# Performance work log

Measured on AMD Instinct MI355X. Metric: run time of the kernel, lower is better.

The kernel has to match this reference:

```python
import jax, jax.numpy as jnp
import numpy as np

NUM_EMBEDDINGS = 1024
EMBEDDING_DIM = 64
COMMIT_COST = 0.25


def setup_inputs() -> dict:
    key = jax.random.key(0)
    k1, k2 = jax.random.split(key)
    latent = jax.random.normal(k1, (32, EMBEDDING_DIM, 32, 32), dtype=jnp.float32)
    embedding_weight = jax.random.normal(k2, (NUM_EMBEDDINGS, EMBEDDING_DIM), dtype=jnp.float32)
    return {"latent": latent, "embedding_weight": embedding_weight}


def reference(latent, embedding_weight):
    # rearrange 'b n j d -> b j d n'; n == embedding_dim
    lat = jnp.transpose(latent, (0, 2, 3, 1))  # [b, j, d, n]
    flat = lat.reshape(-1, EMBEDDING_DIM)      # [T, D]
    # squared-euclidean distances [T, K]
    distances = (
        jnp.sum(flat ** 2, axis=1, keepdims=True)
        + jnp.sum(embedding_weight ** 2, axis=1)
        - 2.0 * flat @ embedding_weight.T
    )
    idx = jnp.argmin(distances, axis=1)                         # [T]
    encodings = jax.nn.one_hot(idx, NUM_EMBEDDINGS, dtype=flat.dtype)  # [T, K]
    quantized_flat = embedding_weight[idx]                      # gather == encodings @ W
    quantized = quantized_flat.reshape(lat.shape)               # [b, j, d, n]

    e_latent_loss = jnp.mean((jax.lax.stop_gradient(quantized) - lat) ** 2)
    loss = COMMIT_COST * e_latent_loss

    # straight-through estimator
    quantized_st = lat + jax.lax.stop_gradient(quantized - lat)

    avg_probs = jnp.mean(encodings, axis=0)
    perplexity = jnp.exp(-jnp.sum(avg_probs * jnp.log(avg_probs + 1e-10)))

    # rearrange back 'b j d n -> b n j d'
    quantized_out = jnp.transpose(quantized_st, (0, 3, 1, 2))
    return quantized_out, loss, perplexity, encodings, distances
```

## Files before the change

### kernel.cpp

```cpp
#include <hip/hip_runtime.h>
#include <cfloat>

#define T_TOTAL 32768
#define DIM 64
#define KCODES 1024

static constexpr long long OFF_Q    = 0;
static constexpr long long OFF_LOSS = 2097152;
static constexpr long long OFF_PERP = 2097153;
static constexpr long long OFF_ENC  = 2097154;
static constexpr long long OFF_DIST = 2097154LL + 33554432LL;


__global__ __launch_bounds__(256) void vq_prep_kernel(const float* __restrict__ W,
                                                      float* __restrict__ ww,
                                                      float* __restrict__ WT) {
    const int tid = threadIdx.x;
    if (blockIdx.x < 256) {
        const int lane = tid & 63;
        const int code = blockIdx.x * 4 + (tid >> 6);
        float v = W[code * DIM + lane];
        float s = v * v;
        #pragma unroll
        for (int off = 32; off > 0; off >>= 1)
            s += __shfl_down(s, off, 64);
        if (lane == 0) ww[code] = s;
    } else {
        const int n = blockIdx.x - 256;
        #pragma unroll
        for (int i = 0; i < 4; ++i) {
            int k = i * 256 + tid;
            WT[n * KCODES + k] = W[k * DIM + n];
        }
    }
}

__global__ __launch_bounds__(256, 3) void vq_main_kernel(const float* __restrict__ lat,
                                                         const float* __restrict__ W,
                                                         const float* __restrict__ ww,
                                                         const float* __restrict__ WT,
                                                         float* __restrict__ out,
                                                         int* __restrict__ counts,
                                                         float* __restrict__ lossSum) {
    __shared__ float xT[64 * 64];
    __shared__ float wS[32 * 256];
    __shared__ float xx[64];
    __shared__ int   selIdx[64];

    const int tid = threadIdx.x;
    const int tx  = tid & 31;
    const int ty  = tid >> 5;
    const int t0  = blockIdx.x * 64;
    const long long base = (long long)(t0 >> 10) * 65536 + (long long)(t0 & 1023);

    #pragma unroll
    for (int i = 0; i < 16; ++i) {
        int e  = i * 256 + tid;
        int n  = e >> 6;
        int tl = e & 63;
        xT[n * 64 + tl] = lat[base + (long long)n * 1024 + tl];
    }
    __syncthreads();
    if (tid < 64) {
        float s = 0.f;
        #pragma unroll 8
        for (int n = 0; n < 64; ++n) {
            float v = xT[n * 64 + tid];
            s = fmaf(v, v, s);
        }
        xx[tid] = s;
    }

    float minV[8];
    int   minI[8];
    #pragma unroll
    for (int r = 0; r < 8; ++r) { minV[r] = FLT_MAX; minI[r] = 0; }

    float* __restrict__ distOut = out + OFF_DIST;

    for (int c = 0; c < 4; ++c) {
        float acc[8][8];
        #pragma unroll
        for (int r = 0; r < 8; ++r)
            #pragma unroll
            for (int k = 0; k < 8; ++k) acc[r][k] = 0.f;

        for (int h = 0; h < 2; ++h) {
            __syncthreads();
            #pragma unroll
            for (int i = 0; i < 8; ++i) {
                int e2 = i * 256 + tid;
                int n  = e2 >> 6;
                int k4 = e2 & 63;
                *(float4*)&wS[n * 256 + k4 * 4] =
                    *(const float4*)&WT[(h * 32 + n) * KCODES + c * 256 + k4 * 4];
            }
            __syncthreads();

            #pragma unroll 4
            for (int nn = 0; nn < 32; ++nn) {
                const float* xrow = &xT[(h * 32 + nn) * 64];
                const float* wrow = &wS[nn * 256];
                float4 a0 = *(const float4*)&xrow[ty * 4];
                float4 a1 = *(const float4*)&xrow[32 + ty * 4];
                float4 b0 = *(const float4*)&wrow[tx * 4];
                float4 b1 = *(const float4*)&wrow[128 + tx * 4];
                float ar[8] = {a0.x, a0.y, a0.z, a0.w, a1.x, a1.y, a1.z, a1.w};
                float br[8] = {b0.x, b0.y, b0.z, b0.w, b1.x, b1.y, b1.z, b1.w};
                #pragma unroll
                for (int r = 0; r < 8; ++r)
                    #pragma unroll
                    for (int k = 0; k < 8; ++k)
                        acc[r][k] = fmaf(ar[r], br[k], acc[r][k]);
            }
        }

        const int kb0 = c * 256 + tx * 4;
        float wr[8];
        #pragma unroll
        for (int k = 0; k < 8; ++k)
            wr[k] = ww[kb0 + (k >> 2) * 128 + (k & 3)];
        #pragma unroll
        for (int r = 0; r < 8; ++r) {
            const int row = (r >> 2) * 32 + ty * 4 + (r & 3);
            const float xxr = xx[row];
            float d[8];
            #pragma unroll
            for (int k = 0; k < 8; ++k) {
                d[k] = (xxr + wr[k]) - 2.f * acc[r][k];
                int ki = kb0 + (k >> 2) * 128 + (k & 3);
                if (d[k] < minV[r]) { minV[r] = d[k]; minI[r] = ki; }
            }
            const long long ro = (long long)(t0 + row) * KCODES + kb0;
            *(float2*)&distOut[ro]           = make_float2(d[0], d[1]);
            *(float2*)&distOut[ro + 2]       = make_float2(d[2], d[3]);
            *(float2*)&distOut[ro + 128]     = make_float2(d[4], d[5]);
            *(float2*)&distOut[ro + 130]     = make_float2(d[6], d[7]);
        }
    }

    __syncthreads();
    float* redV = wS;
    int*   redI = (int*)(wS + 64 * 33);
    #pragma unroll
    for (int r = 0; r < 8; ++r) {
        const int row = (r >> 2) * 32 + ty * 4 + (r & 3);
        redV[row * 33 + tx] = minV[r];
        redI[row * 33 + tx] = minI[r];
    }
    __syncthreads();
    if (tid < 64) {
        float best = redV[tid * 33];
        int   bi   = redI[tid * 33];
        #pragma unroll
        for (int s = 1; s < 32; ++s) {
            float v  = redV[tid * 33 + s];
            int   i2 = redI[tid * 33 + s];
            if (v < best || (v == best && i2 < bi)) { best = v; bi = i2; }
        }
        selIdx[tid] = bi;
        atomicAdd(&counts[bi], 1);
    }
    __syncthreads();

    float* qS = wS;
    #pragma unroll
    for (int i = 0; i < 16; ++i) {
        int e   = i * 256 + tid;
        int row = e >> 6;
        int n   = e & 63;
        qS[row * 65 + n] = W[selIdx[row] * DIM + n];
    }
    __syncthreads();

    float ls = 0.f;
    #pragma unroll
    for (int i = 0; i < 4; ++i) {
        int e2  = i * 256 + tid;
        int n   = e2 >> 4;
        int tl0 = (e2 & 15) * 4;
        float q0 = qS[(tl0 + 0) * 65 + n];
        float q1 = qS[(tl0 + 1) * 65 + n];
        float q2 = qS[(tl0 + 2) * 65 + n];
        float q3 = qS[(tl0 + 3) * 65 + n];
        float x0 = xT[n * 64 + tl0 + 0];
        float x1 = xT[n * 64 + tl0 + 1];
        float x2 = xT[n * 64 + tl0 + 2];
        float x3 = xT[n * 64 + tl0 + 3];
        *(float4*)&out[OFF_Q + base + (long long)n * 1024 + tl0] = make_float4(q0, q1, q2, q3);
        float e0 = q0 - x0; ls = fmaf(e0, e0, ls);
        float e1 = q1 - x1; ls = fmaf(e1, e1, ls);
        float e2d = q2 - x2; ls = fmaf(e2d, e2d, ls);
        float e3 = q3 - x3; ls = fmaf(e3, e3, ls);
    }
    #pragma unroll
    for (int off = 32; off > 0; off >>= 1)
        ls += __shfl_down(ls, off, 64);
    if ((tid & 63) == 0) atomicAdd(lossSum, ls);

    float* __restrict__ enc = out + OFF_ENC;
    for (int i = 0; i < 128; ++i) {
        int e2  = i * 256 + tid;
        int row = e2 >> 9;
        int k2  = (e2 & 511) * 2;
        int sel = selIdx[row];
        float2 v;
        v.x = (k2     == sel) ? 1.f : 0.f;
        v.y = (k2 + 1 == sel) ? 1.f : 0.f;
        *(float2*)&enc[(long long)(t0 + row) * KCODES + k2] = v;
    }
}

__global__ __launch_bounds__(1024) void vq_finalize_kernel(const int* __restrict__ counts,
                                                           const float* __restrict__ lossSum,
                                                           float* __restrict__ out) {
    __shared__ float red[16];
    const int tid = threadIdx.x;
    float p = (float)counts[tid] * (1.0f / 32768.0f);
    float term = p * logf(p + 1e-10f);
    #pragma unroll
    for (int off = 32; off > 0; off >>= 1)
        term += __shfl_down(term, off, 64);
    if ((tid & 63) == 0) red[tid >> 6] = term;
    __syncthreads();
    if (tid == 0) {
        float s = 0.f;
        #pragma unroll
        for (int i = 0; i < 16; ++i) s += red[i];
        out[OFF_PERP] = expf(-s);
        out[OFF_LOSS] = 0.25f * lossSum[0] * (1.0f / 2097152.0f);
    }
}

extern "C" void kernel_launch(void* const* d_in, const int* in_sizes, int n_in,
                              void* d_out, int out_size, void* d_ws, size_t ws_size,
                              hipStream_t stream) {
    (void)in_sizes; (void)n_in; (void)out_size; (void)ws_size;
    const float* lat = (const float*)d_in[0];
    const float* W   = (const float*)d_in[1];
    float* out = (float*)d_out;

    int*   counts  = (int*)d_ws;
    float* ww      = (float*)((char*)d_ws + 4096);
    float* lossSum = (float*)((char*)d_ws + 8192);
    float* WT      = (float*)((char*)d_ws + 12288);

    hipMemsetAsync(d_ws, 0, 8192 + 16, stream);

    vq_prep_kernel<<<320, 256, 0, stream>>>(W, ww, WT);
    vq_main_kernel<<<512, 256, 0, stream>>>(lat, W, ww, WT, out, counts, lossSum);
    vq_finalize_kernel<<<1, 1024, 0, stream>>>(counts, lossSum, out);
}
```

Baseline: 340.2 us.

## Retile VQ main kernel to 32 tokens per block with wave-level argmin

```diff
diff --git a/kernel.cpp b/kernel.cpp
--- a/kernel.cpp
+++ b/kernel.cpp
@@ -35,37 +35,37 @@
     }
 }
 
-__global__ __launch_bounds__(256, 3) void vq_main_kernel(const float* __restrict__ lat,
+__global__ __launch_bounds__(256, 4) void vq_main_kernel(const float* __restrict__ lat,
                                                          const float* __restrict__ W,
                                                          const float* __restrict__ ww,
                                                          const float* __restrict__ WT,
                                                          float* __restrict__ out,
                                                          int* __restrict__ counts,
                                                          float* __restrict__ lossSum) {
-    __shared__ float xT[64 * 64];
-    __shared__ float wS[32 * 256];
-    __shared__ float xx[64];
-    __shared__ int   selIdx[64];
+    __shared__ float xT[64 * 32];
+    __shared__ float wS[8 * 512];
+    __shared__ float xx[32];
+    __shared__ int   selIdx[32];
 
     const int tid = threadIdx.x;
-    const int tx  = tid & 31;
-    const int ty  = tid >> 5;
-    const int t0  = blockIdx.x * 64;
+    const int ct  = tid & 63;
+    const int rg  = tid >> 6;
+    const int t0  = blockIdx.x * 32;
     const long long base = (long long)(t0 >> 10) * 65536 + (long long)(t0 & 1023);
 
     #pragma unroll
-    for (int i = 0; i < 16; ++i) {
+    for (int i = 0; i < 8; ++i) {
         int e  = i * 256 + tid;
-        int n  = e >> 6;
-        int tl = e & 63;
-        xT[n * 64 + tl] = lat[base + (long long)n * 1024 + tl];
-    }
-    __syncthreads();
-    if (tid < 64) {
+        int n  = e >> 5;
+        int tl = e & 31;
+        xT[e] = lat[base + (long long)n * 1024 + tl];
+    }
+    __syncthreads();
+    if (tid < 32) {
         float s = 0.f;
         #pragma unroll 8
         for (int n = 0; n < 64; ++n) {
-            float v = xT[n * 64 + tid];
+            float v = xT[n * 32 + tid];
             s = fmaf(v, v, s);
         }
         xx[tid] = s;
@@ -78,35 +78,36 @@
 
     float* __restrict__ distOut = out + OFF_DIST;
 
-    for (int c = 0; c < 4; ++c) {
+    for (int c = 0; c < 2; ++c) {
         float acc[8][8];
         #pragma unroll
         for (int r = 0; r < 8; ++r)
             #pragma unroll
             for (int k = 0; k < 8; ++k) acc[r][k] = 0.f;
 
-        for (int h = 0; h < 2; ++h) {
+        for (int sub = 0; sub < 8; ++sub) {
             __syncthreads();
             #pragma unroll
-            for (int i = 0; i < 8; ++i) {
-                int e2 = i * 256 + tid;
-                int n  = e2 >> 6;
-                int k4 = e2 & 63;
-                *(float4*)&wS[n * 256 + k4 * 4] =
-                    *(const float4*)&WT[(h * 32 + n) * KCODES + c * 256 + k4 * 4];
+            for (int i = 0; i < 4; ++i) {
+                int e  = i * 256 + tid;
+                int n  = e >> 7;
+                int k4 = (e & 127) * 4;
+                *(float4*)&wS[n * 512 + k4] =
+                    *(const float4*)&WT[(sub * 8 + n) * KCODES + c * 512 + k4];
             }
             __syncthreads();
 
-            #pragma unroll 4
-            for (int nn = 0; nn < 32; ++nn) {
-                const float* xrow = &xT[(h * 32 + nn) * 64];
-                const float* wrow = &wS[nn * 256];
-                float4 a0 = *(const float4*)&xrow[ty * 4];
-                float4 a1 = *(const float4*)&xrow[32 + ty * 4];
-                float4 b0 = *(const float4*)&wrow[tx * 4];
-                float4 b1 = *(const float4*)&wrow[128 + tx * 4];
+            #pragma unroll
+            for (int nn = 0; nn < 8; ++nn) {
+                const int ng = sub * 8 + nn;
+                float4 a0 = *(const float4*)&xT[ng * 32 + rg * 8];
+                float4 a1 = *(const float4*)&xT[ng * 32 + rg * 8 + 4];
+                float2 b0 = *(const float2*)&wS[nn * 512 + ct * 2];
+                float2 b1 = *(const float2*)&wS[nn * 512 + ct * 2 + 128];
+                float2 b2 = *(const float2*)&wS[nn * 512 + ct * 2 + 256];
+                float2 b3 = *(const float2*)&wS[nn * 512 + ct * 2 + 384];
                 float ar[8] = {a0.x, a0.y, a0.z, a0.w, a1.x, a1.y, a1.z, a1.w};
-                float br[8] = {b0.x, b0.y, b0.z, b0.w, b1.x, b1.y, b1.z, b1.w};
+                float br[8] = {b0.x, b0.y, b1.x, b1.y, b2.x, b2.y, b3.x, b3.y};
                 #pragma unroll
                 for (int r = 0; r < 8; ++r)
                     #pragma unroll
@@ -115,57 +116,48 @@
             }
         }
 
-        const int kb0 = c * 256 + tx * 4;
-        float wr[8];
-        #pragma unroll
-        for (int k = 0; k < 8; ++k)
-            wr[k] = ww[kb0 + (k >> 2) * 128 + (k & 3)];
+        const int kb = c * 512 + ct * 2;
+        float2 wwv[4];
+        #pragma unroll
+        for (int j = 0; j < 4; ++j)
+            wwv[j] = *(const float2*)&ww[kb + j * 128];
         #pragma unroll
         for (int r = 0; r < 8; ++r) {
-            const int row = (r >> 2) * 32 + ty * 4 + (r & 3);
+            const int row = rg * 8 + r;
             const float xxr = xx[row];
-            float d[8];
-            #pragma unroll
-            for (int k = 0; k < 8; ++k) {
-                d[k] = (xxr + wr[k]) - 2.f * acc[r][k];
-                int ki = kb0 + (k >> 2) * 128 + (k & 3);
-                if (d[k] < minV[r]) { minV[r] = d[k]; minI[r] = ki; }
+            const long long ro = (long long)(t0 + row) * KCODES + kb;
+            #pragma unroll
+            for (int j = 0; j < 4; ++j) {
+                float d0 = (xxr + wwv[j].x) - 2.f * acc[r][2 * j];
+                float d1 = (xxr + wwv[j].y) - 2.f * acc[r][2 * j + 1];
+                const int ki = kb + j * 128;
+                if (d0 < minV[r]) { minV[r] = d0; minI[r] = ki; }
+                if (d1 < minV[r]) { minV[r] = d1; minI[r] = ki + 1; }
+                *(float2*)&distOut[ro + j * 128] = make_float2(d0, d1);
             }
-            const long long ro = (long long)(t0 + row) * KCODES + kb0;
-            *(float2*)&distOut[ro]           = make_float2(d[0], d[1]);
-            *(float2*)&distOut[ro + 2]       = make_float2(d[2], d[3]);
-            *(float2*)&distOut[ro + 128]     = make_float2(d[4], d[5]);
-            *(float2*)&distOut[ro + 130]     = make_float2(d[6], d[7]);
-        }
-    }
-
-    __syncthreads();
-    float* redV = wS;
-    int*   redI = (int*)(wS + 64 * 33);
+        }
+    }
+
     #pragma unroll
     for (int r = 0; r < 8; ++r) {
-        const int row = (r >> 2) * 32 + ty * 4 + (r & 3);
-        redV[row * 33 + tx] = minV[r];
-        redI[row * 33 + tx] = minI[r];
-    }
-    __syncthreads();
-    if (tid < 64) {
-        float best = redV[tid * 33];
-        int   bi   = redI[tid * 33];
-        #pragma unroll
-        for (int s = 1; s < 32; ++s) {
-            float v  = redV[tid * 33 + s];
-            int   i2 = redI[tid * 33 + s];
-            if (v < best || (v == best && i2 < bi)) { best = v; bi = i2; }
-        }
-        selIdx[tid] = bi;
-        atomicAdd(&counts[bi], 1);
+        float v  = minV[r];
+        int   i0 = minI[r];
+        #pragma unroll
+        for (int off = 32; off > 0; off >>= 1) {
+            float v2 = __shfl_down(v, off, 64);
+            int   i2 = __shfl_down(i0, off, 64);
+            if (v2 < v || (v2 == v && i2 < i0)) { v = v2; i0 = i2; }
+        }
+        if (ct == 0) {
+            selIdx[rg * 8 + r] = i0;
+            atomicAdd(&counts[i0], 1);
+        }
     }
     __syncthreads();
 
     float* qS = wS;
     #pragma unroll
-    for (int i = 0; i < 16; ++i) {
+    for (int i = 0; i < 8; ++i) {
         int e   = i * 256 + tid;
         int row = e >> 6;
         int n   = e & 63;
@@ -175,18 +167,18 @@
 
     float ls = 0.f;
     #pragma unroll
-    for (int i = 0; i < 4; ++i) {
+    for (int i = 0; i < 2; ++i) {
         int e2  = i * 256 + tid;
-        int n   = e2 >> 4;
-        int tl0 = (e2 & 15) * 4;
+        int n   = e2 >> 3;
+        int tl0 = (e2 & 7) * 4;
         float q0 = qS[(tl0 + 0) * 65 + n];
         float q1 = qS[(tl0 + 1) * 65 + n];
         float q2 = qS[(tl0 + 2) * 65 + n];
         float q3 = qS[(tl0 + 3) * 65 + n];
-        float x0 = xT[n * 64 + tl0 + 0];
-        float x1 = xT[n * 64 + tl0 + 1];
-        float x2 = xT[n * 64 + tl0 + 2];
-        float x3 = xT[n * 64 + tl0 + 3];
+        float x0 = xT[n * 32 + tl0 + 0];
+        float x1 = xT[n * 32 + tl0 + 1];
+        float x2 = xT[n * 32 + tl0 + 2];
+        float x3 = xT[n * 32 + tl0 + 3];
         *(float4*)&out[OFF_Q + base + (long long)n * 1024 + tl0] = make_float4(q0, q1, q2, q3);
         float e0 = q0 - x0; ls = fmaf(e0, e0, ls);
         float e1 = q1 - x1; ls = fmaf(e1, e1, ls);
@@ -196,10 +188,11 @@
     #pragma unroll
     for (int off = 32; off > 0; off >>= 1)
         ls += __shfl_down(ls, off, 64);
-    if ((tid & 63) == 0) atomicAdd(lossSum, ls);
+    if (ct == 0) atomicAdd(lossSum, ls);
 
     float* __restrict__ enc = out + OFF_ENC;
-    for (int i = 0; i < 128; ++i) {
+    #pragma unroll 4
+    for (int i = 0; i < 64; ++i) {
         int e2  = i * 256 + tid;
         int row = e2 >> 9;
         int k2  = (e2 & 511) * 2;
@@ -248,6 +241,6 @@
     hipMemsetAsync(d_ws, 0, 8192 + 16, stream);
 
     vq_prep_kernel<<<320, 256, 0, stream>>>(W, ww, WT);
-    vq_main_kernel<<<512, 256, 0, stream>>>(lat, W, ww, WT, out, counts, lossSum);
+    vq_main_kernel<<<1024, 256, 0, stream>>>(lat, W, ww, WT, out, counts, lossSum);
     vq_finalize_kernel<<<1, 1024, 0, stream>>>(counts, lossSum, out);
 }
```

New measurement: 398.9 us. +17.2%, slower.
